# Optimization experiments

Measured on AMD Instinct MI355X. Metric: run time of the kernel, lower is better.

The kernel has to match this reference:

```python
import jax, jax.numpy as jnp
import numpy as np


def _tanh_approx(x):
    return x * jax.lax.rsqrt(1.0 + x * x)


def _lru(u, nu_log, gamma_log, Bm, Cm, Dv):
    # u: [B,T,H]; nu_log/gamma_log: [N]; Bm: [N,H]; Cm: [H,N]; Dv: [H]
    A = jnp.exp(-jnp.exp(nu_log))                       # [N], |A|<1
    Bu = jnp.exp(gamma_log) * jnp.einsum('bth,nh->btn', u, Bm)  # [B,T,N]
    A_full = jnp.broadcast_to(A, Bu.shape)
    # diagonal linear recurrence h_t = A*h_{t-1} + Bu_t via parallel scan
    def comb(c1, c2):
        a1, b1 = c1
        a2, b2 = c2
        return (a1 * a2, a2 * b1 + b2)
    _, h = jax.lax.associative_scan(comb, (A_full, Bu), axis=1)  # inclusive scan
    # module uses the state delayed by one step (out[0]=0, out[t]=h_{t-1})
    h_prev = jnp.pad(h[:, :-1, :], ((0, 0), (1, 0), (0, 0)))
    y = jnp.einsum('btn,hn->bth', h_prev, Cm) + Dv * u
    return y


def _model_block(x, nu_log, gamma_log, Bm, Cm, Dv, Wlin, blin):
    y = _lru(x, nu_log, gamma_log, Bm, Cm, Dv)
    y = _tanh_approx(y) @ Wlin.T + blin
    return y + x


def setup_inputs() -> dict:
    key = jax.random.key(0)
    ks = jax.random.split(key, 10)
    B_, T_, N, H, D = 16, 65536, 64, 64, 4
    r_min, r_max = 0.8, 1.0
    u = jax.random.uniform(ks[0], (D, N))
    nu_log = jnp.log(-0.5 * jnp.log(u * (r_max ** 2 - r_min ** 2) + r_min ** 2))
    A = jnp.exp(-jnp.exp(nu_log))
    gamma_log = jnp.log(jnp.sqrt(1.0 - A ** 2))
    Bm = jax.random.normal(ks[1], (D, N, H)) / np.sqrt(2.0 * H)
    Cm = jax.random.normal(ks[2], (D, H, N)) / np.sqrt(N)
    Dv = jax.random.normal(ks[3], (D, H))
    Wlin = jax.random.normal(ks[4], (D, H, H)) / np.sqrt(H)
    blin = jnp.zeros((D, H))
    Win = jax.random.normal(ks[5], (H, 1))
    Wout = jax.random.normal(ks[6], (1, H)) / np.sqrt(H)
    x = jax.random.normal(ks[7], (B_, T_, 1))
    return {"x": x, "Win": Win, "nu_log": nu_log, "gamma_log": gamma_log,
            "Bm": Bm, "Cm": Cm, "Dv": Dv, "Wlin": Wlin, "blin": blin, "Wout": Wout}


def reference(x, Win, nu_log, gamma_log, Bm, Cm, Dv, Wlin, blin, Wout):
    h = x @ Win.T  # [B,T,H]
    depth = nu_log.shape[0]
    for i in range(depth):
        h = _model_block(h, nu_log[i], gamma_log[i], Bm[i], Cm[i], Dv[i], Wlin[i], blin[i])
    return h @ Wout.T  # [B,T,1]
```

## Files before the change

### kernel.cpp

```cpp
#include <hip/hip_runtime.h>

#define B_ 16
#define T_ 65536
#define H_ 64
#define DEPTH_ 4
#define CHUNK 128
#define NCH (T_ / CHUNK)

typedef _Float16 f16;
typedef f16 f16x8 __attribute__((ext_vector_type(8)));
typedef __fp16 fp16x2 __attribute__((ext_vector_type(2)));
typedef float f32x4 __attribute__((ext_vector_type(4)));
typedef unsigned u32x4 __attribute__((ext_vector_type(4)));

#define MFMA(a, b, c) __builtin_amdgcn_mfma_f32_16x16x32_f16(a, b, c, 0, 0, 0)
#define SWZ(t, k) ((t) * 64 + ((k) ^ (((t) & 7) << 2)))

union U4F8 { u32x4 u; f16x8 h; };

__device__ __forceinline__ f16x8 ldfrag(const f16* p) { return *(const f16x8*)p; }

__device__ __forceinline__ void split8(const float* vv, f16x8* hi, f16x8* lo)
{
    union { f16x8 v; fp16x2 p[4]; } H, L;
    #pragma unroll
    for (int i = 0; i < 4; ++i) {
        fp16x2 h = __builtin_amdgcn_cvt_pkrtz(vv[2 * i], vv[2 * i + 1]);
        H.p[i] = h;
        L.p[i] = __builtin_amdgcn_cvt_pkrtz(vv[2 * i] - (float)h[0],
                                            vv[2 * i + 1] - (float)h[1]);
    }
    *hi = H.v; *lo = L.v;
}

__device__ __forceinline__ f16x8 pack8(const float* vv)
{
    union { f16x8 v; fp16x2 p[4]; } H;
    #pragma unroll
    for (int i = 0; i < 4; ++i)
        H.p[i] = __builtin_amdgcn_cvt_pkrtz(vv[2 * i], vv[2 * i + 1]);
    return H.v;
}

__global__ __launch_bounds__(256)
void prep(const float* __restrict__ Win, const float* __restrict__ nu,
          const float* __restrict__ ga, const float* __restrict__ Bm,
          const float* __restrict__ Cm, const float* __restrict__ Dv,
          const float* __restrict__ Wl,
          f16* __restrict__ BmH, f16* __restrict__ BmL,
          f16* __restrict__ CmH, f16* __restrict__ CmL,
          f16* __restrict__ WlH, float* __restrict__ atab, float* __restrict__ sc)
{
    const int tid = threadIdx.x;
    for (int l = 0; l < DEPTH_; ++l) {
        for (int idx = tid; idx < 4096; idx += 256) {
            int n = idx >> 6;
            float g = expf(ga[l * 64 + n]);
            float v = Bm[l * 4096 + idx] * g;
            f16 h = (f16)v;
            BmH[l * 4096 + idx] = h;
            BmL[l * 4096 + idx] = (f16)(v - (float)h);
            float cv = Cm[l * 4096 + idx];
            h = (f16)cv;
            CmH[l * 4096 + idx] = h;
            CmL[l * 4096 + idx] = (f16)(cv - (float)h);
            WlH[l * 4096 + idx] = (f16)Wl[l * 4096 + idx];
        }
        if (tid < 64) {
            int n = tid;
            float ex = expf(nu[l * 64 + n]);
            float a = expf(-ex);
            float g = expf(ga[l * 64 + n]);
            sc[l * 320 + n] = a;
            sc[l * 320 + 64 + n] = Dv[l * 64 + n];
            float bw = 0.f;
            for (int h2 = 0; h2 < 64; ++h2) bw += Bm[l * 4096 + n * 64 + h2] * Win[h2];
            sc[l * 320 + 128 + n] = bw * g;
            sc[l * 320 + 192 + n] = Dv[l * 64 + n] * Win[n];
            sc[l * 320 + 256 + n] = Win[n];
        }
        for (int idx = tid; idx < 8192; idx += 256) {
            int n = idx >> 7, j = idx & 127;
            float ex = expf(nu[l * 64 + n]);
            atab[l * 8192 + idx] = expf(-ex * (float)j);
        }
    }
}

__global__ __launch_bounds__(64)
void carry_x(const float* __restrict__ x, const float* __restrict__ sc0,
             float* __restrict__ carry)
{
    const int blk = blockIdx.x;
    const int b = blk >> 9, c = blk & (NCH - 1);
    const int n = threadIdx.x;
    const float a  = sc0[n];
    const float bw = sc0[128 + n];
    __shared__ float xs[64];
    const float* xp = x + (size_t)b * T_ + c * CHUNK;
    float s = 0.f;
    for (int bb = 0; bb < CHUNK / 64; ++bb) {
        __syncthreads();
        xs[n] = xp[bb * 64 + n];
        __syncthreads();
        #pragma unroll
        for (int tt = 0; tt < 64; ++tt) s = a * s + bw * xs[tt];
    }
    carry[((size_t)b * NCH + c) * 64 + n] = s;
}

__global__ __launch_bounds__(256)
void scan_carry(const float* __restrict__ nu_log, float* __restrict__ carry)
{
    const int b = blockIdx.x;
    const int tid = threadIdx.x;
    const int n = tid & 63, q = tid >> 6;
    const float ex = expf(nu_log[n]);
    const float aL = expf(-ex * (float)CHUNK);
    float* cp = carry + (size_t)b * NCH * 64 + n;
    __shared__ float part[4][64];

    const int SEG = NCH / 4;
    const int base = q * SEG;
    float p = 0.f;
    #pragma unroll 4
    for (int i = 0; i < SEG; ++i) {
        float v = cp[(size_t)(base + i) * 64];
        cp[(size_t)(base + i) * 64] = p;
        p = aL * p + v;
    }
    part[q][n] = p;
    __syncthreads();
    if (q > 0) {
        const float aLS = expf(-ex * (float)(CHUNK * SEG));
        float inc = 0.f;
        for (int qq = 0; qq < q; ++qq) inc = inc * aLS + part[qq][n];
        float qv = inc;
        #pragma unroll 4
        for (int i = 0; i < SEG; ++i) {
            cp[(size_t)(base + i) * 64] += qv;
            qv *= aL;
        }
    }
}

struct LPrep {
    const f16 *BmH, *BmL, *CmH, *CmL, *WlH;
    const float *av, *dvv, *bw, *dwin, *win;
    const f16 *BmHn, *BmLn;
    const float *atabn;
    const float *blin, *Wout;
};

template<int IN_X, int OUT_FINAL>
__global__ __launch_bounds__(256, 4)
void lru_fused(const float* __restrict__ x, f16* __restrict__ ubuf,
               LPrep P, float* __restrict__ carry, float* __restrict__ out)
{
    const int blk = blockIdx.x;
    const int b = blk >> 9, c = blk & (NCH - 1);
    const int t0 = c * CHUNK;
    const int tid = threadIdx.x;
    const int w = tid >> 6, lane = tid & 63;
    const int l15 = lane & 15, lq = lane >> 4;

    __shared__ float hpk[CHUNK * 64];
    __shared__ float swv[4][64];
    __shared__ float red[4][64];

    f16* ug = ubuf + ((size_t)b * T_ + t0) * 64;
    const float* xg = x + (size_t)b * T_ + t0;

    float cin[4];
    #pragma unroll
    for (int nt = 0; nt < 4; ++nt)
        cin[nt] = carry[((size_t)b * NCH + c) * 64 + nt * 16 + l15];

    f16x8 ahu[2][2];
    if (!IN_X) {
        #pragma unroll
        for (int tt = 0; tt < 2; ++tt) {
            const f16* p = ug + (size_t)((2 * w + tt) * 16 + l15) * 64;
            ahu[tt][0] = ldfrag(p + lq * 8);
            ahu[tt][1] = ldfrag(p + 32 + lq * 8);
        }
    }

    float av4[4];
    #pragma unroll
    for (int nt = 0; nt < 4; ++nt) av4[nt] = P.av[nt * 16 + l15];

    float xv[2][4];
    if (IN_X) {
        #pragma unroll
        for (int tt = 0; tt < 2; ++tt)
            #pragma unroll
            for (int r = 0; r < 4; ++r)
                xv[tt][r] = xg[32 * w + 16 * tt + 4 * lq + r];
    }

    f32x4 acc[4][2];
    if (IN_X) {
        #pragma unroll
        for (int nt = 0; nt < 4; ++nt) {
            float bwn = P.bw[nt * 16 + l15];
            #pragma unroll
            for (int tt = 0; tt < 2; ++tt)
                #pragma unroll
                for (int r = 0; r < 4; ++r) acc[nt][tt][r] = xv[tt][r] * bwn;
        }
    } else {
        #pragma unroll
        for (int nt = 0; nt < 4; ++nt) {
            int n = nt * 16 + l15;
            f16x8 bh0 = ldfrag(P.BmH + n * 64 + lq * 8);
            f16x8 bh1 = ldfrag(P.BmH + n * 64 + 32 + lq * 8);
            f16x8 bl0 = ldfrag(P.BmL + n * 64 + lq * 8);
            f16x8 bl1 = ldfrag(P.BmL + n * 64 + 32 + lq * 8);
            #pragma unroll
            for (int tt = 0; tt < 2; ++tt) {
                f32x4 a4v = {0.f, 0.f, 0.f, 0.f};
                a4v = MFMA(ahu[tt][0], bh0, a4v);
                a4v = MFMA(ahu[tt][0], bl0, a4v);
                a4v = MFMA(ahu[tt][1], bh1, a4v);
                a4v = MFMA(ahu[tt][1], bl1, a4v);
                acc[nt][tt] = a4v;
            }
        }
    }

    float Wb[4][2];
    #pragma unroll
    for (int nt = 0; nt < 4; ++nt) {
        float a = av4[nt], a2 = a * a, a4 = a2 * a2, a8 = a4 * a4, a16 = a8 * a8;
        float P0incl = 0.f;
        #pragma unroll
        for (int tt = 0; tt < 2; ++tt) {
            f32x4 xs = acc[nt][tt];
            float L0 = xs[0];
            float L1 = a * L0 + xs[1];
            float L2 = a * L1 + xs[2];
            float Cv = a * L2 + xs[3];
            float u1 = __shfl_up(Cv, 16);
            float t1 = Cv + ((lq >= 1) ? a4 * u1 : 0.f);
            float u2 = __shfl_up(t1, 32);
            float Pv = t1 + ((lq >= 2) ? a8 * u2 : 0.f);
            float E = __shfl_up(Pv, 16);
            E = (lq == 0) ? 0.f : E;
            if (tt == 0) { Wb[nt][0] = E; P0incl = Pv; }
            else {
                float B0 = __shfl(P0incl, 48 + l15);
                float a4lq = 1.f;
                if (lq & 1) a4lq *= a4;
                if (lq & 2) a4lq *= a8;
                Wb[nt][1] = E + a4lq * B0;
                if (lq == 3) swv[w][nt * 16 + l15] = Pv + a16 * B0;
            }
        }
    }
    __syncthreads();

    #pragma unroll
    for (int nt = 0; nt < 4; ++nt) {
        int n = nt * 16 + l15;
        float a = av4[nt], a2 = a * a, a4 = a2 * a2, a8 = a4 * a4, a16 = a8 * a8, a32 = a16 * a16;
        float inc = cin[nt];
        for (int ww = 0; ww < w; ++ww) inc = inc * a32 + swv[ww][n];
        float a4lq = 1.f;
        if (lq & 1) a4lq *= a4;
        if (lq & 2) a4lq *= a8;
        #pragma unroll
        for (int tt = 0; tt < 2; ++tt) {
            float Z = Wb[nt][tt] + a4lq * (tt ? a16 : 1.f) * inc;
            float s = Z;
            #pragma unroll
            for (int r = 0; r < 4; ++r) {
                int t = 32 * w + 16 * tt + 4 * lq + r;
                hpk[SWZ(t, n)] = s;
                s = a * s + acc[nt][tt][r];
            }
        }
    }

    #pragma unroll
    for (int tt = 0; tt < 2; ++tt) {
        int tb = 2 * w + tt, trow = tb * 16 + l15, sw = (trow & 7) << 2;
        const float* hw = hpk + trow * 64;
        f16x8 ah[2], al[2];
        #pragma unroll
        for (int kk = 0; kk < 2; ++kk) {
            int kb = kk * 32 + lq * 8;
            float4 v0 = *(const float4*)(hw + (kb ^ sw));
            float4 v1 = *(const float4*)(hw + ((kb + 4) ^ sw));
            float vv[8] = {v0.x, v0.y, v0.z, v0.w, v1.x, v1.y, v1.z, v1.w};
            split8(vv, &ah[kk], &al[kk]);
        }
        #pragma unroll
        for (int nt = 0; nt < 4; ++nt) {
            int n = nt * 16 + l15;
            f16x8 ch0 = ldfrag(P.CmH + n * 64 + lq * 8);
            f16x8 ch1 = ldfrag(P.CmH + n * 64 + 32 + lq * 8);
            f16x8 cl0 = ldfrag(P.CmL + n * 64 + lq * 8);
            f16x8 cl1 = ldfrag(P.CmL + n * 64 + 32 + lq * 8);
            f32x4 a4v = {0.f, 0.f, 0.f, 0.f};
            a4v = MFMA(ah[0], ch0, a4v);
            a4v = MFMA(al[0], ch0, a4v);
            a4v = MFMA(ah[0], cl0, a4v);
            a4v = MFMA(ah[1], ch1, a4v);
            a4v = MFMA(al[1], ch1, a4v);
            a4v = MFMA(ah[1], cl1, a4v);
            if (!IN_X) {
                float dv = P.dvv[n];
                f16 dh = (f16)dv, dl = (f16)(dv - (float)dh);
                f16x8 dfh, dfl;
                #pragma unroll
                for (int i2 = 0; i2 < 8; ++i2) { dfh[i2] = (f16)0.f; dfl[i2] = (f16)0.f; }
                int e = ((nt & 1) * 16 + l15) - lq * 8;
                if (e >= 0 && e < 8) { dfh[e] = dh; dfl[e] = dl; }
                a4v = MFMA(ahu[tt][nt >> 1], dfh, a4v);
                a4v = MFMA(ahu[tt][nt >> 1], dfl, a4v);
            }
            float dwin = IN_X ? P.dwin[n] : 0.f;
            #pragma unroll
            for (int r = 0; r < 4; ++r) {
                int t = tb * 16 + lq * 4 + r;
                float y = a4v[r];
                if (IN_X) y += xv[tt][r] * dwin;
                hpk[SWZ(t, n)] = y * rsqrtf(1.f + y * y);
            }
        }
    }

    f16* stg = (f16*)hpk;
    #pragma unroll
    for (int tt = 0; tt < 2; ++tt) {
        int tb = 2 * w + tt, trow = tb * 16 + l15, sw = (trow & 7) << 2;
        const float* hw = hpk + trow * 64;
        f16x8 t0f, t1f;
        #pragma unroll
        for (int kk = 0; kk < 2; ++kk) {
            int kb = kk * 32 + lq * 8;
            float4 v0 = *(const float4*)(hw + (kb ^ sw));
            float4 v1 = *(const float4*)(hw + ((kb + 4) ^ sw));
            float vv[8] = {v0.x, v0.y, v0.z, v0.w, v1.x, v1.y, v1.z, v1.w};
            if (kk == 0) t0f = pack8(vv); else t1f = pack8(vv);
        }
        float val[4] = {0.f, 0.f, 0.f, 0.f};
        #pragma unroll
        for (int nt = 0; nt < 4; ++nt) {
            int n = nt * 16 + l15;
            f16x8 w0f = ldfrag(P.WlH + n * 64 + lq * 8);
            f16x8 w1f = ldfrag(P.WlH + n * 64 + 32 + lq * 8);
            f32x4 a4v = {0.f, 0.f, 0.f, 0.f};
            a4v = MFMA(t0f, w0f, a4v);
            a4v = MFMA(t1f, w1f, a4v);
            if (!IN_X) {
                f16x8 ifr;
                #pragma unroll
                for (int i2 = 0; i2 < 8; ++i2) ifr[i2] = (f16)0.f;
                int e = ((nt & 1) * 16 + l15) - lq * 8;
                if (e >= 0 && e < 8) ifr[e] = (f16)1.f;
                a4v = MFMA(ahu[tt][nt >> 1], ifr, a4v);
            }
            float blj = P.blin[n];
            float wij = IN_X ? P.win[n] : 0.f;
            float woj = OUT_FINAL ? P.Wout[n] : 0.f;
            #pragma unroll
            for (int r = 0; r < 4; ++r) {
                int t = tb * 16 + lq * 4 + r;
                float o = a4v[r] + blj;
                if (IN_X) o += xv[tt][r] * wij;
                if (OUT_FINAL) {
                    val[r] += o * woj;
                } else {
                    int g = n >> 1;
                    int word = t * 64 + (((g & ~3) ^ ((t & 7) << 2)) | (g & 3));
                    stg[word * 2 + (n & 1)] = (f16)o;
                }
            }
        }
        if (OUT_FINAL) {
            #pragma unroll
            for (int r = 0; r < 4; ++r) {
                float p = val[r];
                p += __shfl_xor(p, 1);
                p += __shfl_xor(p, 2);
                p += __shfl_xor(p, 4);
                p += __shfl_xor(p, 8);
                if (l15 == 0) out[(size_t)b * T_ + t0 + tb * 16 + lq * 4 + r] = p;
            }
        }
    }

    if (!OUT_FINAL) {
        #pragma unroll
        for (int i = 0; i < 4; ++i) {
            int row = 32 * w + i * 8 + (lane >> 3);
            int gg = 4 * (lane & 7);
            int word = row * 64 + (gg ^ ((row & 7) << 2));
            u32x4 cv = *(const u32x4*)(hpk + word);
            *(u32x4*)(ug + (size_t)row * 64 + 8 * (lane & 7)) = cv;
        }

        float partial[4] = {0.f, 0.f, 0.f, 0.f};
        #pragma unroll
        for (int tt = 0; tt < 2; ++tt) {
            int tb = 2 * w + tt, arow = tb * 16 + l15, msk = (arow & 7) << 2;
            U4F8 av0, av1;
            av0.u = *(const u32x4*)(hpk + arow * 64 + ((4 * lq) ^ msk));
            av1.u = *(const u32x4*)(hpk + arow * 64 + ((16 + 4 * lq) ^ msk));
            #pragma unroll
            for (int nt = 0; nt < 4; ++nt) {
                int n = nt * 16 + l15;
                f16x8 bh0 = ldfrag(P.BmHn + n * 64 + lq * 8);
                f16x8 bh1 = ldfrag(P.BmHn + n * 64 + 32 + lq * 8);
                f16x8 bl0 = ldfrag(P.BmLn + n * 64 + lq * 8);
                f16x8 bl1 = ldfrag(P.BmLn + n * 64 + 32 + lq * 8);
                f32x4 a4v = {0.f, 0.f, 0.f, 0.f};
                a4v = MFMA(av0.h, bh0, a4v);
                a4v = MFMA(av0.h, bl0, a4v);
                a4v = MFMA(av1.h, bh1, a4v);
                a4v = MFMA(av1.h, bl1, a4v);
                float4 dp = *(const float4*)(P.atabn + n * 128 + 124 - tb * 16 - lq * 4);
                partial[nt] += a4v[0] * dp.w + a4v[1] * dp.z + a4v[2] * dp.y + a4v[3] * dp.x;
            }
        }
        #pragma unroll
        for (int nt = 0; nt < 4; ++nt) {
            float v = partial[nt];
            v += __shfl_xor(v, 16);
            v += __shfl_xor(v, 32);
            if (lq == 0) red[w][nt * 16 + l15] = v;
        }
        __syncthreads();
        if (w == 0)
            carry[((size_t)b * NCH + c) * 64 + lane] =
                red[0][lane] + red[1][lane] + red[2][lane] + red[3][lane];
    }
}

extern "C" void kernel_launch(void* const* d_in, const int* in_sizes, int n_in,
                              void* d_out, int out_size, void* d_ws, size_t ws_size,
                              hipStream_t stream)
{
    const float* x   = (const float*)d_in[0];
    const float* Win = (const float*)d_in[1];
    const float* nu  = (const float*)d_in[2];
    const float* ga  = (const float*)d_in[3];
    const float* Bm  = (const float*)d_in[4];
    const float* Cm  = (const float*)d_in[5];
    const float* Dv  = (const float*)d_in[6];
    const float* Wl  = (const float*)d_in[7];
    const float* bl  = (const float*)d_in[8];
    const float* Wo  = (const float*)d_in[9];
    float* out = (float*)d_out;

    char* p = (char*)d_ws;
    f16* ubuf = (f16*)p;            p += (size_t)B_ * T_ * 64 * sizeof(f16);
    float* carry = (float*)p;       p += (size_t)B_ * NCH * 64 * sizeof(float);
    f16* wBmH = (f16*)p;            p += 4 * 4096 * sizeof(f16);
    f16* wBmL = (f16*)p;            p += 4 * 4096 * sizeof(f16);
    f16* wCmH = (f16*)p;            p += 4 * 4096 * sizeof(f16);
    f16* wCmL = (f16*)p;            p += 4 * 4096 * sizeof(f16);
    f16* wWlH = (f16*)p;            p += 4 * 4096 * sizeof(f16);
    float* atab = (float*)p;        p += 4 * 8192 * sizeof(float);
    float* sc = (float*)p;          p += 4 * 320 * sizeof(float);

    dim3 grid(B_ * NCH), blk256(256), blk64(64), gscan(B_);

    prep<<<1, 256, 0, stream>>>(Win, nu, ga, Bm, Cm, Dv, Wl,
                                wBmH, wBmL, wCmH, wCmL, wWlH, atab, sc);
    carry_x<<<grid, blk64, 0, stream>>>(x, sc, carry);

    for (int l = 0; l < DEPTH_; ++l) {
        int ln = (l + 1 < DEPTH_) ? l + 1 : l;
        scan_carry<<<gscan, blk256, 0, stream>>>(nu + l * 64, carry);
        LPrep Pr;
        Pr.BmH = wBmH + l * 4096;  Pr.BmL = wBmL + l * 4096;
        Pr.CmH = wCmH + l * 4096;  Pr.CmL = wCmL + l * 4096;
        Pr.WlH = wWlH + l * 4096;
        Pr.av = sc + l * 320;       Pr.dvv = sc + l * 320 + 64;
        Pr.bw = sc + l * 320 + 128; Pr.dwin = sc + l * 320 + 192;
        Pr.win = sc + l * 320 + 256;
        Pr.BmHn = wBmH + ln * 4096; Pr.BmLn = wBmL + ln * 4096;
        Pr.atabn = atab + ln * 8192;
        Pr.blin = bl + l * 64; Pr.Wout = Wo;
        if (l == 0)
            lru_fused<1, 0><<<grid, blk256, 0, stream>>>(x, ubuf, Pr, carry, out);
        else if (l == DEPTH_ - 1)
            lru_fused<0, 1><<<grid, blk256, 0, stream>>>(x, ubuf, Pr, carry, out);
        else
            lru_fused<0, 0><<<grid, blk256, 0, stream>>>(x, ubuf, Pr, carry, out);
    }
}
```

Baseline: 1.393 ms.

## Switch carry granularity to per-wave 32-step chunks, removing intra-block carry exchange

Chunk carries are now kept at 32-timestep granularity, one per wave, instead of one per 128-step block. Each wave reads its own incoming carry directly and writes its outgoing carry contribution without a shared-memory reduction, which removes two __syncthreads and the cross-wave prefix in the fused kernel. In exchange, the carry buffer and the sequential scan_carry work grow fourfold (now 512 threads and 8 segments per batch), the carry_x grid is four times larger, and the decay table shrinks to 32 entries.

```diff
diff --git a/kernel.cpp b/kernel.cpp
--- a/kernel.cpp
+++ b/kernel.cpp
@@ -5,7 +5,9 @@
 #define H_ 64
 #define DEPTH_ 4
 #define CHUNK 128
-#define NCH (T_ / CHUNK)
+#define CHW 32
+#define NCHW (T_ / CHW)
+#define NCHB (T_ / CHUNK)
 
 typedef _Float16 f16;
 typedef f16 f16x8 __attribute__((ext_vector_type(8)));
@@ -79,10 +81,10 @@
             sc[l * 320 + 192 + n] = Dv[l * 64 + n] * Win[n];
             sc[l * 320 + 256 + n] = Win[n];
         }
-        for (int idx = tid; idx < 8192; idx += 256) {
-            int n = idx >> 7, j = idx & 127;
+        for (int idx = tid; idx < 2048; idx += 256) {
+            int n = idx >> 5, j = idx & 31;
             float ex = expf(nu[l * 64 + n]);
-            atab[l * 8192 + idx] = expf(-ex * (float)j);
+            atab[l * 2048 + idx] = expf(-ex * (float)j);
         }
     }
 }
@@ -92,35 +94,32 @@
              float* __restrict__ carry)
 {
     const int blk = blockIdx.x;
-    const int b = blk >> 9, c = blk & (NCH - 1);
+    const int b = blk >> 11, c = blk & (NCHW - 1);
     const int n = threadIdx.x;
     const float a  = sc0[n];
     const float bw = sc0[128 + n];
-    __shared__ float xs[64];
-    const float* xp = x + (size_t)b * T_ + c * CHUNK;
+    __shared__ float xs[CHW];
+    const float* xp = x + (size_t)b * T_ + c * CHW;
+    if (n < CHW) xs[n] = xp[n];
+    __syncthreads();
     float s = 0.f;
-    for (int bb = 0; bb < CHUNK / 64; ++bb) {
-        __syncthreads();
-        xs[n] = xp[bb * 64 + n];
-        __syncthreads();
-        #pragma unroll
-        for (int tt = 0; tt < 64; ++tt) s = a * s + bw * xs[tt];
-    }
-    carry[((size_t)b * NCH + c) * 64 + n] = s;
-}
-
-__global__ __launch_bounds__(256)
+    #pragma unroll
+    for (int tt = 0; tt < CHW; ++tt) s = a * s + bw * xs[tt];
+    carry[((size_t)b * NCHW + c) * 64 + n] = s;
+}
+
+__global__ __launch_bounds__(512)
 void scan_carry(const float* __restrict__ nu_log, float* __restrict__ carry)
 {
     const int b = blockIdx.x;
     const int tid = threadIdx.x;
     const int n = tid & 63, q = tid >> 6;
     const float ex = expf(nu_log[n]);
-    const float aL = expf(-ex * (float)CHUNK);
-    float* cp = carry + (size_t)b * NCH * 64 + n;
-    __shared__ float part[4][64];
-
-    const int SEG = NCH / 4;
+    const float aL = expf(-ex * (float)CHW);
+    float* cp = carry + (size_t)b * NCHW * 64 + n;
+    __shared__ float part[8][64];
+
+    const int SEG = NCHW / 8;
     const int base = q * SEG;
     float p = 0.f;
     #pragma unroll 4
@@ -132,7 +131,7 @@
     part[q][n] = p;
     __syncthreads();
     if (q > 0) {
-        const float aLS = expf(-ex * (float)(CHUNK * SEG));
+        const float aLS = expf(-ex * (float)(CHW * SEG));
         float inc = 0.f;
         for (int qq = 0; qq < q; ++qq) inc = inc * aLS + part[qq][n];
         float qv = inc;
@@ -158,15 +157,14 @@
                LPrep P, float* __restrict__ carry, float* __restrict__ out)
 {
     const int blk = blockIdx.x;
-    const int b = blk >> 9, c = blk & (NCH - 1);
-    const int t0 = c * CHUNK;
+    const int b = blk >> 9, cblk = blk & (NCHB - 1);
+    const int t0 = cblk * CHUNK;
     const int tid = threadIdx.x;
     const int w = tid >> 6, lane = tid & 63;
     const int l15 = lane & 15, lq = lane >> 4;
+    const int cw = cblk * 4 + w;
 
     __shared__ float hpk[CHUNK * 64];
-    __shared__ float swv[4][64];
-    __shared__ float red[4][64];
 
     f16* ug = ubuf + ((size_t)b * T_ + t0) * 64;
     const float* xg = x + (size_t)b * T_ + t0;
@@ -174,7 +172,7 @@
     float cin[4];
     #pragma unroll
     for (int nt = 0; nt < 4; ++nt)
-        cin[nt] = carry[((size_t)b * NCH + c) * 64 + nt * 16 + l15];
+        cin[nt] = carry[((size_t)b * NCHW + cw) * 64 + nt * 16 + l15];
 
     f16x8 ahu[2][2];
     if (!IN_X) {
@@ -232,7 +230,7 @@
     float Wb[4][2];
     #pragma unroll
     for (int nt = 0; nt < 4; ++nt) {
-        float a = av4[nt], a2 = a * a, a4 = a2 * a2, a8 = a4 * a4, a16 = a8 * a8;
+        float a = av4[nt], a2 = a * a, a4 = a2 * a2, a8 = a4 * a4;
         float P0incl = 0.f;
         #pragma unroll
         for (int tt = 0; tt < 2; ++tt) {
@@ -254,18 +252,15 @@
                 if (lq & 1) a4lq *= a4;
                 if (lq & 2) a4lq *= a8;
                 Wb[nt][1] = E + a4lq * B0;
-                if (lq == 3) swv[w][nt * 16 + l15] = Pv + a16 * B0;
-            }
-        }
-    }
-    __syncthreads();
+            }
+        }
+    }
 
     #pragma unroll
     for (int nt = 0; nt < 4; ++nt) {
         int n = nt * 16 + l15;
-        float a = av4[nt], a2 = a * a, a4 = a2 * a2, a8 = a4 * a4, a16 = a8 * a8, a32 = a16 * a16;
+        float a = av4[nt], a2 = a * a, a4 = a2 * a2, a8 = a4 * a4, a16 = a8 * a8;
         float inc = cin[nt];
-        for (int ww = 0; ww < w; ++ww) inc = inc * a32 + swv[ww][n];
         float a4lq = 1.f;
         if (lq & 1) a4lq *= a4;
         if (lq & 2) a4lq *= a8;
@@ -421,7 +416,7 @@
                 a4v = MFMA(av0.h, bl0, a4v);
                 a4v = MFMA(av1.h, bh1, a4v);
                 a4v = MFMA(av1.h, bl1, a4v);
-                float4 dp = *(const float4*)(P.atabn + n * 128 + 124 - tb * 16 - lq * 4);
+                float4 dp = *(const float4*)(P.atabn + n * 32 + 28 - tt * 16 - lq * 4);
                 partial[nt] += a4v[0] * dp.w + a4v[1] * dp.z + a4v[2] * dp.y + a4v[3] * dp.x;
             }
         }
@@ -430,12 +425,9 @@
             float v = partial[nt];
             v += __shfl_xor(v, 16);
             v += __shfl_xor(v, 32);
-            if (lq == 0) red[w][nt * 16 + l15] = v;
-        }
-        __syncthreads();
-        if (w == 0)
-            carry[((size_t)b * NCH + c) * 64 + lane] =
-                red[0][lane] + red[1][lane] + red[2][lane] + red[3][lane];
+            if (lq == 0)
+                carry[((size_t)b * NCHW + cw) * 64 + nt * 16 + l15] = v;
+        }
     }
 }
 
@@ -457,24 +449,24 @@
 
     char* p = (char*)d_ws;
     f16* ubuf = (f16*)p;            p += (size_t)B_ * T_ * 64 * sizeof(f16);
-    float* carry = (float*)p;       p += (size_t)B_ * NCH * 64 * sizeof(float);
+    float* carry = (float*)p;       p += (size_t)B_ * NCHW * 64 * sizeof(float);
     f16* wBmH = (f16*)p;            p += 4 * 4096 * sizeof(f16);
     f16* wBmL = (f16*)p;            p += 4 * 4096 * sizeof(f16);
     f16* wCmH = (f16*)p;            p += 4 * 4096 * sizeof(f16);
     f16* wCmL = (f16*)p;            p += 4 * 4096 * sizeof(f16);
     f16* wWlH = (f16*)p;            p += 4 * 4096 * sizeof(f16);
-    float* atab = (float*)p;        p += 4 * 8192 * sizeof(float);
+    float* atab = (float*)p;        p += 4 * 2048 * sizeof(float);
     float* sc = (float*)p;          p += 4 * 320 * sizeof(float);
 
-    dim3 grid(B_ * NCH), blk256(256), blk64(64), gscan(B_);
+    dim3 gfused(B_ * NCHB), gcarry(B_ * NCHW), blk512(512), blk256(256), blk64(64), gscan(B_);
 
     prep<<<1, 256, 0, stream>>>(Win, nu, ga, Bm, Cm, Dv, Wl,
                                 wBmH, wBmL, wCmH, wCmL, wWlH, atab, sc);
-    carry_x<<<grid, blk64, 0, stream>>>(x, sc, carry);
+    carry_x<<<gcarry, blk64, 0, stream>>>(x, sc, carry);
 
     for (int l = 0; l < DEPTH_; ++l) {
         int ln = (l + 1 < DEPTH_) ? l + 1 : l;
-        scan_carry<<<gscan, blk256, 0, stream>>>(nu + l * 64, carry);
+        scan_carry<<<gscan, blk512, 0, stream>>>(nu + l * 64, carry);
         LPrep Pr;
         Pr.BmH = wBmH + l * 4096;  Pr.BmL = wBmL + l * 4096;
         Pr.CmH = wCmH + l * 4096;  Pr.CmL = wCmL + l * 4096;
@@ -483,13 +475,13 @@
         Pr.bw = sc + l * 320 + 128; Pr.dwin = sc + l * 320 + 192;
         Pr.win = sc + l * 320 + 256;
         Pr.BmHn = wBmH + ln * 4096; Pr.BmLn = wBmL + ln * 4096;
-        Pr.atabn = atab + ln * 8192;
+        Pr.atabn = atab + ln * 2048;
         Pr.blin = bl + l * 64; Pr.Wout = Wo;
         if (l == 0)
-            lru_fused<1, 0><<<grid, blk256, 0, stream>>>(x, ubuf, Pr, carry, out);
+            lru_fused<1, 0><<<gfused, blk256, 0, stream>>>(x, ubuf, Pr, carry, out);
         else if (l == DEPTH_ - 1)
-            lru_fused<0, 1><<<grid, blk256, 0, stream>>>(x, ubuf, Pr, carry, out);
+            lru_fused<0, 1><<<gfused, blk256, 0, stream>>>(x, ubuf, Pr, carry, out);
         else
-            lru_fused<0, 0><<<grid, blk256, 0, stream>>>(x, ubuf, Pr, carry, out);
-    }
-}
+            lru_fused<0, 0><<<gfused, blk256, 0, stream>>>(x, ubuf, Pr, carry, out);
+    }
+}
```

Result: slower. 1.472 ms (+5.7%).
